# Kernel tuning notes

Hardware: AMD Instinct MI355X
Metric: run time of the kernel (lower is better)

The kernel has to match this reference:

```python
import jax, jax.numpy as jnp
import numpy as np

C_T, C_Z, C_HID, N_HEADS = 64, 128, 16, 4
N_TEMPL, N_RES = 4, 512
INF = 1e9


def setup_inputs() -> dict:
    key = jax.random.key(0)
    ks = jax.random.split(key, 7)
    return {
        "t": jax.random.normal(ks[0], (N_TEMPL, N_RES, N_RES, C_T), jnp.float32),
        "z": jax.random.normal(ks[1], (N_RES, N_RES, C_Z), jnp.float32),
        "template_mask": jnp.ones((N_TEMPL,), jnp.float32),
        "wq": jax.random.normal(ks[2], (C_Z, N_HEADS * C_HID), jnp.float32) * 0.05,
        "wk": jax.random.normal(ks[3], (C_T, N_HEADS * C_HID), jnp.float32) * 0.05,
        "wv": jax.random.normal(ks[4], (C_T, N_HEADS * C_HID), jnp.float32) * 0.05,
        "wo": jax.random.normal(ks[5], (N_HEADS * C_HID, C_Z), jnp.float32) * 0.05,
        "bo": jnp.zeros((C_Z,), jnp.float32),
    }


def reference(t, z, template_mask, wq, wk, wv, wo, bo):
    # t: [S, N, N, C_t]  z: [N, N, C_z]  template_mask: [S]
    h, d = N_HEADS, C_HID
    bias = INF * (template_mask - 1.0)  # [S], 0 for kept, -inf for masked
    tp = jnp.transpose(t, (1, 2, 0, 3))  # [N, N, S, C_t] (permute_final_dims (1,2,0,3))
    scale = 1.0 / jnp.sqrt(jnp.asarray(d, z.dtype))
    q = jnp.einsum("ijc,chd->ijhd", z, wq.reshape(C_Z, h, d)) * scale  # [N,N,h,d]
    k = jnp.einsum("ijsc,chd->ijshd", tp, wk.reshape(C_T, h, d))       # [N,N,S,h,d]
    v = jnp.einsum("ijsc,chd->ijshd", tp, wv.reshape(C_T, h, d))
    logits = jnp.einsum("ijhd,ijshd->ijhs", q, k) + bias  # [N,N,h,S]
    a = jax.nn.softmax(logits, axis=-1)
    o = jnp.einsum("ijhs,ijshd->ijhd", a, v).reshape(N_RES, N_RES, h * d)
    out = o @ wo + bo  # [N, N, C_z]
    out = out * (jnp.sum(template_mask) > 0).astype(out.dtype)
    return out
```

## Files before the change

kernel.cpp:

```cpp
#include <hip/hip_runtime.h>

#define NRES 512
#define CZ   128
#define CT   64

typedef short bf16x8 __attribute__((ext_vector_type(8)));
typedef float f32x4  __attribute__((ext_vector_type(4)));

#define MFMA16(a,b,c) __builtin_amdgcn_mfma_f32_16x16x32_bf16((a),(b),(c),0,0,0)

__device__ __forceinline__ unsigned short f2bf(float f){
  unsigned int u = __builtin_bit_cast(unsigned int, f);
  u += 0x7fffu + ((u >> 16) & 1u);
  return (unsigned short)(u >> 16);
}
__device__ __forceinline__ bf16x8 pack8(const float4 a, const float4 b){
  bf16x8 r;
  r[0]=(short)f2bf(a.x); r[1]=(short)f2bf(a.y); r[2]=(short)f2bf(a.z); r[3]=(short)f2bf(a.w);
  r[4]=(short)f2bf(b.x); r[5]=(short)f2bf(b.y); r[6]=(short)f2bf(b.z); r[7]=(short)f2bf(b.w);
  return r;
}

template<int CTRL>
__device__ __forceinline__ float dppadd(float x){
  int y = __builtin_amdgcn_update_dpp(0, __builtin_bit_cast(int, x), CTRL, 0xF, 0xF, false);
  return x + __builtin_bit_cast(float, y);
}
__device__ __forceinline__ f32x4 reduce16(f32x4 p){
#pragma unroll
  for (int r = 0; r < 4; ++r){
    float v = p[r];
    v = dppadd<0xB1>(v);
    v = dppadd<0x4E>(v);
    v = dppadd<0x141>(v);
    v = dppadd<0x140>(v);
    p[r] = v;
  }
  return p;
}

__global__ void prep_pack(const float* __restrict__ wq, const float* __restrict__ wk,
                          const float* __restrict__ wv, const float* __restrict__ wo,
                          unsigned short* __restrict__ packed){
  int idx = blockIdx.x * 256 + threadIdx.x;
  if (idx >= 48 * 64) return;
  int f = idx >> 6, lane = idx & 63;
  const float* W; int Ncols, nt, ks; float scale = 1.0f;
  if (f < 16)      { W = wq; Ncols = 64;  nt = f >> 2;        ks = f & 3;        scale = 0.25f; }
  else if (f < 24) { W = wk; Ncols = 64;  nt = (f - 16) >> 1; ks = (f - 16) & 1; }
  else if (f < 32) { W = wv; Ncols = 64;  nt = (f - 24) >> 1; ks = (f - 24) & 1; }
  else             { W = wo; Ncols = 128; nt = (f - 32) >> 1; ks = (f - 32) & 1; }
  int col = nt * 16 + (lane & 15);
  int k0  = ks * 32 + (lane >> 4) * 8;
  unsigned short* dst = packed + (size_t)f * 512 + (size_t)lane * 8;
#pragma unroll
  for (int j = 0; j < 8; ++j)
    dst[j] = f2bf(W[(k0 + j) * Ncols + col] * scale);
}

__launch_bounds__(512, 4)
__global__ void tpa_main(const float* __restrict__ t, const float* __restrict__ z,
                         const float* __restrict__ mask, const float* __restrict__ bo,
                         const unsigned short* __restrict__ packed,
                         float* __restrict__ out){
  __shared__ __align__(16) char smem[49152];

  const int tid  = threadIdx.x;
  const int lane = tid & 63;
  const int w    = tid >> 6;
  const int cl   = lane & 15;
  const int g    = lane >> 4;
  const int b    = blockIdx.x;
  const int i    = b >> 2;
  const int j0   = (b & 3) << 7;
  const int r0   = j0 + (w << 4);
  const int grow = r0 + cl;

  {
#pragma unroll
    for (int it = 0; it < 6; ++it){
      int idx = it * 512 + tid;
      __builtin_amdgcn_global_load_lds(
          reinterpret_cast<const uint4*>(packed) + idx,
          reinterpret_cast<uint4*>(smem) + idx, 16, 0, 0);
    }
  }

  const float4* zp = reinterpret_cast<const float4*>(z + ((size_t)i * NRES + grow) * CZ);
  bf16x8 za[4];
#pragma unroll
  for (int ks = 0; ks < 4; ++ks){
    float4 p0 = zp[ks * 8 + g * 2 + 0];
    float4 p1 = zp[ks * 8 + g * 2 + 1];
    za[ks] = pack8(p0, p1);
  }

  bf16x8 ta[4][2];
#pragma unroll
  for (int s = 0; s < 4; ++s){
    const float4* tp4 = reinterpret_cast<const float4*>(
        t + (((size_t)s * NRES + i) * NRES + grow) * CT);
    float4 a0 = tp4[g * 2 + 0];
    float4 a1 = tp4[g * 2 + 1];
    float4 a2 = tp4[8 + g * 2 + 0];
    float4 a3 = tp4[8 + g * 2 + 1];
    ta[s][0] = pack8(a0, a1);
    ta[s][1] = pack8(a2, a3);
  }

  float m0 = mask[0], m1 = mask[1], m2 = mask[2], m3 = mask[3];
  float msum = m0 + m1 + m2 + m3;
  float bias[4] = {1e9f * (m0 - 1.0f), 1e9f * (m1 - 1.0f),
                   1e9f * (m2 - 1.0f), 1e9f * (m3 - 1.0f)};

  __syncthreads();

#define LDB(fi) (*reinterpret_cast<const bf16x8*>(smem + (size_t)(fi) * 1024 + (size_t)lane * 16))

  f32x4 qf[4];
#pragma unroll
  for (int h = 0; h < 4; ++h){
    f32x4 q = {0.f, 0.f, 0.f, 0.f};
#pragma unroll
    for (int ks = 0; ks < 4; ++ks) q = MFMA16(za[ks], LDB(h * 4 + ks), q);
    qf[h] = q;
  }

  __syncthreads();

  unsigned short* o_ws = reinterpret_cast<unsigned short*>(smem + w * 2048);

#pragma unroll
  for (int h = 0; h < 4; ++h){
    f32x4 lgh[4];
#pragma unroll
    for (int s = 0; s < 4; ++s){
      f32x4 acc = {0.f, 0.f, 0.f, 0.f};
      acc = MFMA16(ta[s][0], LDB(16 + h * 2 + 0), acc);
      acc = MFMA16(ta[s][1], LDB(16 + h * 2 + 1), acc);
      f32x4 p = reduce16(acc * qf[h]);
#pragma unroll
      for (int r = 0; r < 4; ++r) p[r] += bias[s];
      lgh[s] = p;
    }
    f32x4 mx, sum = {0.f, 0.f, 0.f, 0.f};
#pragma unroll
    for (int r = 0; r < 4; ++r)
      mx[r] = fmaxf(fmaxf(lgh[0][r], lgh[1][r]), fmaxf(lgh[2][r], lgh[3][r]));
#pragma unroll
    for (int s = 0; s < 4; ++s){
#pragma unroll
      for (int r = 0; r < 4; ++r) lgh[s][r] = __expf(lgh[s][r] - mx[r]);
      sum += lgh[s];
    }
    f32x4 inv;
#pragma unroll
    for (int r = 0; r < 4; ++r) inv[r] = 1.0f / sum[r];
#pragma unroll
    for (int s = 0; s < 4; ++s) lgh[s] *= inv;

    f32x4 of = {0.f, 0.f, 0.f, 0.f};
#pragma unroll
    for (int s = 0; s < 4; ++s){
      f32x4 vacc = {0.f, 0.f, 0.f, 0.f};
      vacc = MFMA16(ta[s][0], LDB(24 + h * 2 + 0), vacc);
      vacc = MFMA16(ta[s][1], LDB(24 + h * 2 + 1), vacc);
      of += lgh[s] * vacc;
    }
#pragma unroll
    for (int r = 0; r < 4; ++r){
      int row = (g << 2) + r;
      o_ws[row * 64 + ((h * 16 + cl) ^ ((row & 7) << 3))] = (unsigned short)f2bf(of[r]);
    }
  }
  asm volatile("s_waitcnt lgkmcnt(0)" ::: "memory");

  {
    bf16x8 oa[2];
#pragma unroll
    for (int ks = 0; ks < 2; ++ks)
      oa[ks] = *reinterpret_cast<const bf16x8*>(
          o_ws + cl * 64 + ((ks * 32 + g * 8) ^ ((cl & 7) << 3)));

    float gate = (msum > 0.0f) ? 1.0f : 0.0f;
    float* outg = out + ((size_t)i * NRES + r0) * CZ;
#pragma unroll
    for (int nt = 0; nt < 8; ++nt){
      f32x4 acc = {0.f, 0.f, 0.f, 0.f};
      acc = MFMA16(oa[0], LDB(32 + nt * 2 + 0), acc);
      acc = MFMA16(oa[1], LDB(32 + nt * 2 + 1), acc);
      int col = nt * 16 + cl;
      float bov = bo[col];
#pragma unroll
      for (int r = 0; r < 4; ++r)
        outg[(size_t)((g << 2) + r) * CZ + col] = (acc[r] + bov) * gate;
    }
  }
}

extern "C" void kernel_launch(void* const* d_in, const int* in_sizes, int n_in,
                              void* d_out, int out_size, void* d_ws, size_t ws_size,
                              hipStream_t stream) {
  const float* t    = (const float*)d_in[0];
  const float* z    = (const float*)d_in[1];
  const float* mask = (const float*)d_in[2];
  const float* wq   = (const float*)d_in[3];
  const float* wk   = (const float*)d_in[4];
  const float* wv   = (const float*)d_in[5];
  const float* wo   = (const float*)d_in[6];
  const float* bo   = (const float*)d_in[7];
  unsigned short* packed = (unsigned short*)d_ws;

  hipLaunchKernelGGL(prep_pack, dim3(12), dim3(256), 0, stream, wq, wk, wv, wo, packed);
  hipLaunchKernelGGL(tpa_main, dim3(2048), dim3(512), 0, stream,
                     t, z, mask, bo, packed, (float*)d_out);
}
```

Before: 114.9 us.

## Make main kernel persistent over four row tiles with prefetched template loads

```diff
diff --git a/kernel.cpp b/kernel.cpp
--- a/kernel.cpp
+++ b/kernel.cpp
@@ -58,12 +58,13 @@
     dst[j] = f2bf(W[(k0 + j) * Ncols + col] * scale);
 }
 
-__launch_bounds__(512, 4)
+#define WLDS 49152
+__launch_bounds__(256, 3)
 __global__ void tpa_main(const float* __restrict__ t, const float* __restrict__ z,
                          const float* __restrict__ mask, const float* __restrict__ bo,
                          const unsigned short* __restrict__ packed,
                          float* __restrict__ out){
-  __shared__ __align__(16) char smem[49152];
+  __shared__ __align__(16) char smem[54272];
 
   const int tid  = threadIdx.x;
   const int lane = tid & 63;
@@ -71,124 +72,147 @@
   const int cl   = lane & 15;
   const int g    = lane >> 4;
   const int b    = blockIdx.x;
-  const int i    = b >> 2;
-  const int j0   = (b & 3) << 7;
-  const int r0   = j0 + (w << 4);
-  const int grow = r0 + cl;
-
+  const int i    = b >> 1;
+  const int jb   = (b & 1) << 8;
+
+  unsigned short* oh = reinterpret_cast<unsigned short*>(smem + WLDS + w * 1280);
+
+  float4 traw[16];
   {
-#pragma unroll
-    for (int it = 0; it < 6; ++it){
-      int idx = it * 512 + tid;
-      __builtin_amdgcn_global_load_lds(
-          reinterpret_cast<const uint4*>(packed) + idx,
-          reinterpret_cast<uint4*>(smem) + idx, 16, 0, 0);
-    }
-  }
-
-  const float4* zp = reinterpret_cast<const float4*>(z + ((size_t)i * NRES + grow) * CZ);
-  bf16x8 za[4];
-#pragma unroll
-  for (int ks = 0; ks < 4; ++ks){
-    float4 p0 = zp[ks * 8 + g * 2 + 0];
-    float4 p1 = zp[ks * 8 + g * 2 + 1];
-    za[ks] = pack8(p0, p1);
-  }
-
-  bf16x8 ta[4][2];
-#pragma unroll
-  for (int s = 0; s < 4; ++s){
-    const float4* tp4 = reinterpret_cast<const float4*>(
-        t + (((size_t)s * NRES + i) * NRES + grow) * CT);
-    float4 a0 = tp4[g * 2 + 0];
-    float4 a1 = tp4[g * 2 + 1];
-    float4 a2 = tp4[8 + g * 2 + 0];
-    float4 a3 = tp4[8 + g * 2 + 1];
-    ta[s][0] = pack8(a0, a1);
-    ta[s][1] = pack8(a2, a3);
-  }
-
-  float m0 = mask[0], m1 = mask[1], m2 = mask[2], m3 = mask[3];
-  float msum = m0 + m1 + m2 + m3;
-  float bias[4] = {1e9f * (m0 - 1.0f), 1e9f * (m1 - 1.0f),
-                   1e9f * (m2 - 1.0f), 1e9f * (m3 - 1.0f)};
+    const int grow0 = jb + (w << 4) + cl;
+#pragma unroll
+    for (int s = 0; s < 4; ++s){
+      const float4* tp4 = reinterpret_cast<const float4*>(
+          t + (((size_t)s * NRES + i) * NRES + grow0) * CT);
+      traw[s * 4 + 0] = tp4[g * 2 + 0];
+      traw[s * 4 + 1] = tp4[g * 2 + 1];
+      traw[s * 4 + 2] = tp4[8 + g * 2 + 0];
+      traw[s * 4 + 3] = tp4[8 + g * 2 + 1];
+    }
+  }
+
+#pragma unroll
+  for (int it = 0; it < 12; ++it){
+    int idx = it * 256 + tid;
+    __builtin_amdgcn_global_load_lds(
+        reinterpret_cast<const uint4*>(packed) + idx,
+        reinterpret_cast<uint4*>(smem) + idx, 16, 0, 0);
+  }
+
+  const float m0 = mask[0], m1 = mask[1], m2 = mask[2], m3 = mask[3];
+  const float msum = m0 + m1 + m2 + m3;
+  const float gate = (msum > 0.0f) ? 1.0f : 0.0f;
+  const float bias[4] = {1e9f * (m0 - 1.0f), 1e9f * (m1 - 1.0f),
+                         1e9f * (m2 - 1.0f), 1e9f * (m3 - 1.0f)};
 
   __syncthreads();
 
 #define LDB(fi) (*reinterpret_cast<const bf16x8*>(smem + (size_t)(fi) * 1024 + (size_t)lane * 16))
 
-  f32x4 qf[4];
-#pragma unroll
-  for (int h = 0; h < 4; ++h){
-    f32x4 q = {0.f, 0.f, 0.f, 0.f};
-#pragma unroll
-    for (int ks = 0; ks < 4; ++ks) q = MFMA16(za[ks], LDB(h * 4 + ks), q);
-    qf[h] = q;
-  }
-
-  __syncthreads();
-
-  unsigned short* o_ws = reinterpret_cast<unsigned short*>(smem + w * 2048);
-
-#pragma unroll
-  for (int h = 0; h < 4; ++h){
-    f32x4 lgh[4];
+#pragma unroll 1
+  for (int tt = 0; tt < 4; ++tt){
+    const int j0   = jb + (tt << 6);
+    const int grow = j0 + (w << 4) + cl;
+
+    const float4* zp = reinterpret_cast<const float4*>(z + ((size_t)i * NRES + grow) * CZ);
+    float4 zr[8];
+#pragma unroll
+    for (int ks = 0; ks < 4; ++ks){
+      zr[ks * 2 + 0] = zp[ks * 8 + g * 2 + 0];
+      zr[ks * 2 + 1] = zp[ks * 8 + g * 2 + 1];
+    }
+
+    bf16x8 ta[4][2];
 #pragma unroll
     for (int s = 0; s < 4; ++s){
-      f32x4 acc = {0.f, 0.f, 0.f, 0.f};
-      acc = MFMA16(ta[s][0], LDB(16 + h * 2 + 0), acc);
-      acc = MFMA16(ta[s][1], LDB(16 + h * 2 + 1), acc);
-      f32x4 p = reduce16(acc * qf[h]);
-#pragma unroll
-      for (int r = 0; r < 4; ++r) p[r] += bias[s];
-      lgh[s] = p;
-    }
-    f32x4 mx, sum = {0.f, 0.f, 0.f, 0.f};
-#pragma unroll
-    for (int r = 0; r < 4; ++r)
-      mx[r] = fmaxf(fmaxf(lgh[0][r], lgh[1][r]), fmaxf(lgh[2][r], lgh[3][r]));
-#pragma unroll
-    for (int s = 0; s < 4; ++s){
-#pragma unroll
-      for (int r = 0; r < 4; ++r) lgh[s][r] = __expf(lgh[s][r] - mx[r]);
-      sum += lgh[s];
-    }
-    f32x4 inv;
-#pragma unroll
-    for (int r = 0; r < 4; ++r) inv[r] = 1.0f / sum[r];
-#pragma unroll
-    for (int s = 0; s < 4; ++s) lgh[s] *= inv;
-
-    f32x4 of = {0.f, 0.f, 0.f, 0.f};
-#pragma unroll
-    for (int s = 0; s < 4; ++s){
-      f32x4 vacc = {0.f, 0.f, 0.f, 0.f};
-      vacc = MFMA16(ta[s][0], LDB(24 + h * 2 + 0), vacc);
-      vacc = MFMA16(ta[s][1], LDB(24 + h * 2 + 1), vacc);
-      of += lgh[s] * vacc;
-    }
-#pragma unroll
-    for (int r = 0; r < 4; ++r){
-      int row = (g << 2) + r;
-      o_ws[row * 64 + ((h * 16 + cl) ^ ((row & 7) << 3))] = (unsigned short)f2bf(of[r]);
-    }
-  }
-  asm volatile("s_waitcnt lgkmcnt(0)" ::: "memory");
-
-  {
-    bf16x8 oa[2];
-#pragma unroll
-    for (int ks = 0; ks < 2; ++ks)
-      oa[ks] = *reinterpret_cast<const bf16x8*>(
-          o_ws + cl * 64 + ((ks * 32 + g * 8) ^ ((cl & 7) << 3)));
-
-    float gate = (msum > 0.0f) ? 1.0f : 0.0f;
-    float* outg = out + ((size_t)i * NRES + r0) * CZ;
+      ta[s][0] = pack8(traw[s * 4 + 0], traw[s * 4 + 1]);
+      ta[s][1] = pack8(traw[s * 4 + 2], traw[s * 4 + 3]);
+    }
+
+    if (tt < 3){
+      const int grown = grow + 64;
+#pragma unroll
+      for (int s = 0; s < 4; ++s){
+        const float4* tp4 = reinterpret_cast<const float4*>(
+            t + (((size_t)s * NRES + i) * NRES + grown) * CT);
+        traw[s * 4 + 0] = tp4[g * 2 + 0];
+        traw[s * 4 + 1] = tp4[g * 2 + 1];
+        traw[s * 4 + 2] = tp4[8 + g * 2 + 0];
+        traw[s * 4 + 3] = tp4[8 + g * 2 + 1];
+      }
+    }
+
+    bf16x8 za[4];
+#pragma unroll
+    for (int ks = 0; ks < 4; ++ks)
+      za[ks] = pack8(zr[ks * 2], zr[ks * 2 + 1]);
+
+    f32x4 qf[4];
+#pragma unroll
+    for (int h = 0; h < 4; ++h){
+      f32x4 q = {0.f, 0.f, 0.f, 0.f};
+#pragma unroll
+      for (int ks = 0; ks < 4; ++ks) q = MFMA16(za[ks], LDB(h * 4 + ks), q);
+      qf[h] = q;
+    }
+
+    bf16x8 oa0, oa1;
+#pragma unroll
+    for (int h = 0; h < 4; ++h){
+      f32x4 lgh[4];
+#pragma unroll
+      for (int s = 0; s < 4; ++s){
+        f32x4 acc = {0.f, 0.f, 0.f, 0.f};
+        acc = MFMA16(ta[s][0], LDB(16 + h * 2 + 0), acc);
+        acc = MFMA16(ta[s][1], LDB(16 + h * 2 + 1), acc);
+        f32x4 p = reduce16(acc * qf[h]);
+#pragma unroll
+        for (int r = 0; r < 4; ++r) p[r] += bias[s];
+        lgh[s] = p;
+      }
+      f32x4 mx, sum = {0.f, 0.f, 0.f, 0.f};
+#pragma unroll
+      for (int r = 0; r < 4; ++r)
+        mx[r] = fmaxf(fmaxf(lgh[0][r], lgh[1][r]), fmaxf(lgh[2][r], lgh[3][r]));
+#pragma unroll
+      for (int s = 0; s < 4; ++s){
+#pragma unroll
+        for (int r = 0; r < 4; ++r) lgh[s][r] = __expf(lgh[s][r] - mx[r]);
+        sum += lgh[s];
+      }
+      f32x4 inv;
+#pragma unroll
+      for (int r = 0; r < 4; ++r) inv[r] = 1.0f / sum[r];
+#pragma unroll
+      for (int s = 0; s < 4; ++s) lgh[s] *= inv;
+
+      f32x4 of = {0.f, 0.f, 0.f, 0.f};
+#pragma unroll
+      for (int s = 0; s < 4; ++s){
+        f32x4 vacc = {0.f, 0.f, 0.f, 0.f};
+        vacc = MFMA16(ta[s][0], LDB(24 + h * 2 + 0), vacc);
+        vacc = MFMA16(ta[s][1], LDB(24 + h * 2 + 1), vacc);
+        of += lgh[s] * vacc;
+      }
+      const int h2 = h & 1;
+#pragma unroll
+      for (int r = 0; r < 4; ++r)
+        oh[(g * 4 + r) * 40 + h2 * 16 + cl] = f2bf(of[r]);
+      if (h == 1){
+        asm volatile("s_waitcnt lgkmcnt(0)" ::: "memory");
+        oa0 = *reinterpret_cast<const bf16x8*>(oh + cl * 40 + g * 8);
+        asm volatile("s_waitcnt lgkmcnt(0)" ::: "memory");
+      }
+    }
+    asm volatile("s_waitcnt lgkmcnt(0)" ::: "memory");
+    oa1 = *reinterpret_cast<const bf16x8*>(oh + cl * 40 + g * 8);
+
+    float* outg = out + ((size_t)i * NRES + j0 + (w << 4)) * CZ;
 #pragma unroll
     for (int nt = 0; nt < 8; ++nt){
       f32x4 acc = {0.f, 0.f, 0.f, 0.f};
-      acc = MFMA16(oa[0], LDB(32 + nt * 2 + 0), acc);
-      acc = MFMA16(oa[1], LDB(32 + nt * 2 + 1), acc);
+      acc = MFMA16(oa0, LDB(32 + nt * 2 + 0), acc);
+      acc = MFMA16(oa1, LDB(32 + nt * 2 + 1), acc);
       int col = nt * 16 + cl;
       float bov = bo[col];
 #pragma unroll
@@ -212,6 +236,6 @@
   unsigned short* packed = (unsigned short*)d_ws;
 
   hipLaunchKernelGGL(prep_pack, dim3(12), dim3(256), 0, stream, wq, wk, wv, wo, packed);
-  hipLaunchKernelGGL(tpa_main, dim3(2048), dim3(512), 0, stream,
+  hipLaunchKernelGGL(tpa_main, dim3(1024), dim3(256), 0, stream,
                      t, z, mask, bo, packed, (float*)d_out);
 }
```

After: 172.2 us. 49.9% more time.
